# Kernel tuning notes

Hardware: AMD Instinct MI355X
Metric: run time of the kernel (lower is better)

The kernel has to match this reference:

```python
import jax, jax.numpy as jnp
import numpy as np

NC, NV = 1, 256
DE, D, DA = 512, 512, 512
KS = (2, 4, 4)
STRIDE = (2, 4, 4)
BLOCK = (4, 8, 8)
NHEAD = 8
NLAYERS = 2
PAD = -1
N_SLICE = STRIDE[0] * STRIDE[1] * STRIDE[2]  # 32


def _block_local_attention(x, wq, wk, wv, wo, block, n_head):
    # x: (b, d, T, H, W); non-overlapping block-local multi-head self-attention
    b, d, T, H, W = x.shape
    bt, bh, bw = block
    nt, nh, nw = T // bt, H // bh, W // bw
    L = bt * bh * bw
    da = wq.shape[1]
    hd = da // n_head
    # partition grid into blocks -> (b*nblocks, L, d)
    xs = x.transpose(0, 2, 3, 4, 1)                      # (b,T,H,W,d)
    xs = xs.reshape(b, nt, bt, nh, bh, nw, bw, d)
    xs = xs.transpose(0, 1, 3, 5, 2, 4, 6, 7).reshape(b * nt * nh * nw, L, d)
    q = (xs @ wq).reshape(-1, L, n_head, hd)
    k = (xs @ wk).reshape(-1, L, n_head, hd)
    v = (xs @ wv).reshape(-1, L, n_head, hd)
    scores = jnp.einsum('nqhd,nkhd->nhqk', q, k) / jnp.sqrt(jnp.float32(hd))
    attn = jax.nn.softmax(scores, axis=-1)
    o = jnp.einsum('nhqk,nkhd->nqhd', attn, v).reshape(-1, L, da)
    out = xs + o @ wo                                    # residual
    out = out.reshape(b, nt, nh, nw, bt, bh, bw, d)
    out = out.transpose(0, 1, 4, 2, 5, 3, 6, 7).reshape(b, T, H, W, d)
    return out.transpose(0, 4, 1, 2, 3)


def setup_inputs() -> dict:
    key = jax.random.key(0)
    ks = jax.random.split(key, 10)
    s = 0.02
    x = jax.random.randint(ks[0], (4, NC, 16, 64, 64), 0, NV)
    slice_idx = jax.random.randint(ks[1], (4,), 0, N_SLICE)
    conv_w = jax.random.normal(ks[2], (DE, NC * NV, *KS), jnp.float32) * s
    conv_b = jax.random.normal(ks[3], (DE,), jnp.float32) * s
    slice_emb = jax.random.normal(ks[4], (N_SLICE, DE), jnp.float32) * s
    proj_w = jax.random.normal(ks[5], (D, DE), jnp.float32) * s
    attn_wq = jax.random.normal(ks[6], (NLAYERS, D, DA), jnp.float32) * s
    attn_wk = jax.random.normal(ks[7], (NLAYERS, D, DA), jnp.float32) * s
    attn_wv = jax.random.normal(ks[8], (NLAYERS, D, DA), jnp.float32) * s
    attn_wo = jax.random.normal(ks[9], (NLAYERS, DA, D), jnp.float32) * s
    return {"x": x, "slice_idx": slice_idx, "conv_w": conv_w, "conv_b": conv_b,
            "slice_emb": slice_emb, "proj_w": proj_w, "attn_wq": attn_wq,
            "attn_wk": attn_wk, "attn_wv": attn_wv, "attn_wo": attn_wo}


def reference(x, slice_idx, conv_w, conv_b, slice_emb, proj_w,
              attn_wq, attn_wk, attn_wv, attn_wo):
    mask = x == PAD                                        # (b,nc,T,H,W)
    xt = jnp.where(mask, 0, x)
    oh = jax.nn.one_hot(xt, NV, dtype=jnp.float32)         # (b,nc,T,H,W,nv)
    oh = oh * (~mask)[..., None].astype(jnp.float32)
    b, nc, T, H, W, nv = oh.shape
    h = oh.transpose(0, 1, 5, 2, 3, 4).reshape(b, nc * nv, T, H, W)
    h = jax.lax.conv_general_dilated(h, conv_w, STRIDE, 'VALID',
                                     dimension_numbers=('NCDHW', 'OIDHW', 'NCDHW'))
    h = h + conv_b[None, :, None, None, None]
    h = h + slice_emb[slice_idx][:, :, None, None, None]
    h = jnp.einsum('bcthw,dc->bdthw', h, proj_w)           # 1x1x1 conv, no bias
    for i in range(NLAYERS):
        h = _block_local_attention(h, attn_wq[i], attn_wk[i], attn_wv[i],
                                   attn_wo[i], BLOCK, NHEAD)
    return h
```

## Files before the change

### kernel.cpp

```cpp
#include <hip/hip_runtime.h>
#include <hip/hip_bf16.h>

typedef unsigned short u16x8 __attribute__((ext_vector_type(8)));
typedef unsigned int u32x4 __attribute__((ext_vector_type(4)));
typedef __bf16 bf16x8 __attribute__((ext_vector_type(8)));
typedef float f32x4 __attribute__((ext_vector_type(4)));
typedef float f32x16 __attribute__((ext_vector_type(16)));

#define NTAP 32
#define NROWS 8192

__device__ inline unsigned short bf16bits(float f) {
  __hip_bfloat16 hb = __float2bfloat16(f);
  return __builtin_bit_cast(unsigned short, hb);
}
__device__ inline unsigned int pk2(float lo, float hi) {
  return (unsigned int)bf16bits(lo) | ((unsigned int)bf16bits(hi) << 16);
}
__device__ inline float bf2f(unsigned short u) {
  return __builtin_bit_cast(float, (unsigned int)u << 16);
}

__global__ void k_prepconv(const float* __restrict__ src, unsigned short* __restrict__ dst) {
  __shared__ float tile[64][65];
  int vt0 = blockIdx.x * 64, de0 = blockIdx.y * 64;
  int t = threadIdx.x;
#pragma unroll
  for (int p = 0; p < 16; p++) {
    int r = p * 4 + (t >> 6), c = t & 63;
    tile[r][c] = src[(size_t)(de0 + r) * 8192 + vt0 + c];
  }
  __syncthreads();
#pragma unroll
  for (int p = 0; p < 16; p++) {
    int r = p * 4 + (t >> 6), c = t & 63;
    dst[(size_t)(vt0 + r) * 512 + de0 + c] = bf16bits(tile[c][r]);
  }
}

__global__ void k_prepw(const float* __restrict__ proj_w, const float* __restrict__ wq,
                        const float* __restrict__ wk, const float* __restrict__ wv,
                        const float* __restrict__ wo, unsigned short* __restrict__ Wb) {
  __shared__ float tile[64][65];
  int mat = blockIdx.z;
  int n0 = blockIdx.x * 64, k0 = blockIdx.y * 64;
  int t = threadIdx.x;
  unsigned short* dst = Wb + (size_t)mat * 262144;
  if (mat == 0) {
#pragma unroll
    for (int p = 0; p < 16; p++) {
      int r = p * 4 + (t >> 6), c = t & 63;
      dst[(size_t)(n0 + r) * 512 + k0 + c] = bf16bits(proj_w[(size_t)(n0 + r) * 512 + k0 + c]);
    }
  } else {
    int idx = mat - 1, comp = idx & 3, L = idx >> 2;
    const float* srcs[4] = {wq, wk, wv, wo};
    const float* src = srcs[comp] + (size_t)L * 262144;
#pragma unroll
    for (int p = 0; p < 16; p++) {
      int r = p * 4 + (t >> 6), c = t & 63;
      tile[r][c] = src[(size_t)(k0 + r) * 512 + n0 + c];
    }
    __syncthreads();
#pragma unroll
    for (int p = 0; p < 16; p++) {
      int r = p * 4 + (t >> 6), c = t & 63;
      dst[(size_t)(n0 + r) * 512 + k0 + c] = bf16bits(tile[c][r]);
    }
  }
}

__global__ void k_embed(const int* __restrict__ x, const int* __restrict__ slice_idx,
                        const unsigned short* __restrict__ wTb, const float* __restrict__ conv_b,
                        const float* __restrict__ slice_emb, unsigned short* __restrict__ H0b) {
  int tid = threadIdx.x;
  int g = tid >> 6, l = tid & 63;
  int r = blockIdx.x * 4 + g;
  int blk = r >> 8, ll = r & 255;
  int bw = blk & 1, bh = (blk >> 1) & 1, bt = (blk >> 2) & 1, b = blk >> 3;
  int lw = ll & 7, lh = (ll >> 3) & 7, lt = ll >> 6;
  int t = bt * 4 + lt, h = bh * 8 + lh, w = bw * 8 + lw;

  __shared__ int toks[4][NTAP];
  if (l < NTAP) {
    int kt = l >> 4, kh = (l >> 2) & 3, kw = l & 3;
    toks[g][l] = x[((b * 16 + (2 * t + kt)) * 64 + (4 * h + kh)) * 64 + (4 * w + kw)];
  }
  __syncthreads();
  int sl = slice_idx[b];
  float4 cb0 = *(const float4*)&conv_b[l * 8];
  float4 cb1 = *(const float4*)&conv_b[l * 8 + 4];
  float4 se0 = *(const float4*)&slice_emb[sl * 512 + l * 8];
  float4 se1 = *(const float4*)&slice_emb[sl * 512 + l * 8 + 4];
  float acc[8] = {cb0.x + se0.x, cb0.y + se0.y, cb0.z + se0.z, cb0.w + se0.w,
                  cb1.x + se1.x, cb1.y + se1.y, cb1.z + se1.z, cb1.w + se1.w};
  for (int tap = 0; tap < NTAP; tap++) {
    int v = toks[g][tap];
    if (v >= 0) {
      u16x8 wv = *(const u16x8*)&wTb[(size_t)(v * NTAP + tap) * 512 + l * 8];
#pragma unroll
      for (int j = 0; j < 8; j++) acc[j] += bf2f(wv[j]);
    }
  }
  u16x8 o;
#pragma unroll
  for (int j = 0; j < 8; j++) o[j] = bf16bits(acc[j]);
  *(u16x8*)&H0b[(size_t)r * 512 + l * 8] = o;
}

template <int WM, bool RES>
__global__ void __launch_bounds__(256)
k_gemm_mfma(const unsigned short* __restrict__ A, const unsigned short* __restrict__ B,
            float* __restrict__ Cf, unsigned short* __restrict__ Cb,
            unsigned short* __restrict__ Vt) {
  __shared__ __align__(16) unsigned short As[128 * 64];
  __shared__ __align__(16) unsigned short Bs[128 * 64];
  int m0 = blockIdx.x * 128, n0 = blockIdx.y * 128;
  int tid = threadIdx.x;
  int lane = tid & 63, wid = tid >> 6;
  int wr = wid >> 1, wc = wid & 1;
  int l15 = lane & 15, lgrp = lane >> 4;
  int srow = tid >> 3, sx = tid & 7;
  f32x4 acc[4][4] = {};
  for (int k0 = 0; k0 < 512; k0 += 64) {
    u16x8 ra[4], rb[4];
#pragma unroll
    for (int i = 0; i < 4; i++) {
      int row = i * 32 + srow;
      int c = sx ^ (row & 7);
      ra[i] = *(const u16x8*)&A[(size_t)(m0 + row) * 512 + k0 + c * 8];
      rb[i] = *(const u16x8*)&B[(size_t)(n0 + row) * 512 + k0 + c * 8];
    }
    __syncthreads();
#pragma unroll
    for (int i = 0; i < 4; i++) {
      int row = i * 32 + srow;
      *(u16x8*)&As[row * 64 + sx * 8] = ra[i];
      *(u16x8*)&Bs[row * 64 + sx * 8] = rb[i];
    }
    __syncthreads();
#pragma unroll
    for (int kk = 0; kk < 2; kk++) {
      bf16x8 a[4], b[4];
#pragma unroll
      for (int m = 0; m < 4; m++) {
        int row = wr * 64 + m * 16 + l15;
        int xx = (kk * 4 + lgrp) ^ (row & 7);
        a[m] = __builtin_bit_cast(bf16x8, *(const u16x8*)&As[row * 64 + xx * 8]);
      }
#pragma unroll
      for (int n = 0; n < 4; n++) {
        int row = wc * 64 + n * 16 + l15;
        int xx = (kk * 4 + lgrp) ^ (row & 7);
        b[n] = __builtin_bit_cast(bf16x8, *(const u16x8*)&Bs[row * 64 + xx * 8]);
      }
#pragma unroll
      for (int m = 0; m < 4; m++)
#pragma unroll
        for (int n = 0; n < 4; n++)
          acc[m][n] = __builtin_amdgcn_mfma_f32_16x16x32_bf16(a[m], b[n], acc[m][n], 0, 0, 0);
    }
  }
#pragma unroll
  for (int m = 0; m < 4; m++) {
#pragma unroll
    for (int n = 0; n < 4; n++) {
      int gcol = n0 + wc * 64 + n * 16 + l15;
#pragma unroll
      for (int r = 0; r < 4; r++) {
        int grow = m0 + wr * 64 + m * 16 + lgrp * 4 + r;
        float v = acc[m][n][r];
        if (WM == 1) {
          if (RES) v += Cf[(size_t)grow * 512 + gcol];
          Cf[(size_t)grow * 512 + gcol] = v;
          Cb[(size_t)grow * 512 + gcol] = bf16bits(v);
        } else {
          if (gcol < 1024) Cb[(size_t)grow * 1024 + gcol] = bf16bits(v);
          else Vt[(size_t)(gcol - 1024) * 8192 + grow] = bf16bits(v);
        }
      }
    }
  }
}

__global__ void __launch_bounds__(256)
k_attn_mfma(const unsigned short* __restrict__ QKb, const unsigned short* __restrict__ Vt,
            unsigned short* __restrict__ O16) {
  __shared__ __align__(16) unsigned short Ks[256 * 64];
  __shared__ __align__(16) unsigned short Vs[64 * 256];
  int bid = blockIdx.x >> 3, head = blockIdx.x & 7;
  int r0 = bid * 256;
  int tid = threadIdx.x, lane = tid & 63, wid = tid >> 6;
  {
    int key = tid >> 3, j = tid & 7;
#pragma unroll
    for (int p = 0; p < 8; p++) {
      int k2 = key + p * 32;
      u16x8 v = *(const u16x8*)&QKb[(size_t)(r0 + k2) * 1024 + 512 + head * 64 + j * 8];
      *(u16x8*)&Ks[k2 * 64 + ((j ^ (k2 & 7)) * 8)] = v;
    }
    int dv = tid >> 2, sg = tid & 3;
    const unsigned short* src = &Vt[(size_t)(head * 64 + dv) * 8192 + r0 + sg * 64];
#pragma unroll
    for (int c = 0; c < 8; c++) {
      u16x8 v = *(const u16x8*)&src[c * 8];
      int ch = sg * 8 + c;
      *(u16x8*)&Vs[dv * 256 + ((ch ^ (dv & 7)) * 8)] = v;
    }
  }
  int l31 = lane & 31, hi = lane >> 5;
  int qb = wid * 64;
  bf16x8 qfrag[2][4];
#pragma unroll
  for (int g = 0; g < 2; g++)
#pragma unroll
    for (int s = 0; s < 4; s++)
      qfrag[g][s] = __builtin_bit_cast(
          bf16x8, *(const u16x8*)&QKb[(size_t)(r0 + qb + g * 32 + l31) * 1024 + head * 64 +
                                      s * 16 + hi * 8]);
  __syncthreads();

  f32x16 oacc[2][2] = {};
  float mx[2] = {-1e30f, -1e30f}, lsum[2] = {0.f, 0.f};

  for (int kt = 0; kt < 8; kt++) {
    bf16x8 kfrag[4];
    int key = kt * 32 + l31;
#pragma unroll
    for (int s = 0; s < 4; s++) {
      int j = s * 2 + hi;
      kfrag[s] = __builtin_bit_cast(bf16x8, *(const u16x8*)&Ks[key * 64 + ((j ^ (key & 7)) * 8)]);
    }
#pragma unroll
    for (int g = 0; g < 2; g++) {
      f32x16 sacc = {};
#pragma unroll
      for (int s = 0; s < 4; s++)
        sacc = __builtin_amdgcn_mfma_f32_32x32x16_bf16(kfrag[s], qfrag[g][s], sacc, 0, 0, 0);
      float tmax = sacc[0];
#pragma unroll
      for (int r = 1; r < 16; r++) tmax = fmaxf(tmax, sacc[r]);
      tmax = fmaxf(tmax, __shfl_xor(tmax, 32, 64));
      float mn = fmaxf(mx[g], tmax);
      float sc = __expf((mx[g] - mn) * 0.125f);
      float p[16], ts = 0.f;
#pragma unroll
      for (int r = 0; r < 16; r++) {
        p[r] = __expf((sacc[r] - mn) * 0.125f);
        ts += p[r];
      }
      ts += __shfl_xor(ts, 32, 64);
      lsum[g] = lsum[g] * sc + ts;
      mx[g] = mn;
#pragma unroll
      for (int dvt = 0; dvt < 2; dvt++)
#pragma unroll
        for (int r = 0; r < 16; r++) oacc[g][dvt][r] *= sc;
#pragma unroll
      for (int st = 0; st < 2; st++) {
        unsigned int A = pk2(p[st * 8 + 0], p[st * 8 + 1]);
        unsigned int Bw = pk2(p[st * 8 + 2], p[st * 8 + 3]);
        unsigned int C = pk2(p[st * 8 + 4], p[st * 8 + 5]);
        unsigned int D = pk2(p[st * 8 + 6], p[st * 8 + 7]);
        asm volatile("v_permlane32_swap_b32 %0, %1" : "+v"(A), "+v"(C));
        asm volatile("v_permlane32_swap_b32 %0, %1" : "+v"(Bw), "+v"(D));
        u32x4 fw = {A, Bw, C, D};
        bf16x8 pfrag = __builtin_bit_cast(bf16x8, fw);
#pragma unroll
        for (int dvt = 0; dvt < 2; dvt++) {
          int dv = dvt * 32 + l31;
          int ch = kt * 4 + st * 2 + hi;
          bf16x8 vfrag = __builtin_bit_cast(
              bf16x8, *(const u16x8*)&Vs[dv * 256 + ((ch ^ (dv & 7)) * 8)]);
          oacc[g][dvt] = __builtin_amdgcn_mfma_f32_32x32x16_bf16(vfrag, pfrag, oacc[g][dvt], 0, 0, 0);
        }
      }
    }
  }
#pragma unroll
  for (int g = 0; g < 2; g++) {
    float inv = 1.f / lsum[g];
    size_t rowb = (size_t)(r0 + qb + g * 32 + l31) * 512 + head * 64;
#pragma unroll
    for (int dvt = 0; dvt < 2; dvt++)
#pragma unroll
      for (int r = 0; r < 16; r += 2) {
        int dv = dvt * 32 + (r & 3) + 8 * (r >> 2) + 4 * hi;
        unsigned int po = pk2(oacc[g][dvt][r] * inv, oacc[g][dvt][r + 1] * inv);
        *(unsigned int*)&O16[rowb + dv] = po;
      }
  }
}

__global__ void k_writeout(const float* __restrict__ H, float* __restrict__ out) {
  __shared__ float t[512][33];
  int bp = blockIdx.x;
  int d0 = blockIdx.y * 32;
  int tid = threadIdx.x;
  int base_row = bp * 512;
#pragma unroll
  for (int i = 0; i < 16; i++) {
    int id = i * 256 + tid;
    int r = id >> 3, c = id & 7;
    float4 v = *(const float4*)&H[(size_t)(base_row + r) * 512 + d0 + c * 4];
    t[r][c * 4 + 0] = v.x;
    t[r][c * 4 + 1] = v.y;
    t[r][c * 4 + 2] = v.z;
    t[r][c * 4 + 3] = v.w;
  }
  __syncthreads();
  int b = bp >> 2, bt = (bp >> 1) & 1, bh = bp & 1;
  int w = tid & 15, lh = (tid >> 4) & 7, ltl = tid >> 7;
  int lw = w & 7, bw = w >> 3;
#pragma unroll
  for (int dd = 0; dd < 32; dd++) {
#pragma unroll
    for (int s = 0; s < 2; s++) {
      int lt = s * 2 + ltl;
      int pos = bw * 256 + lt * 64 + lh * 8 + lw;
      out[((size_t)(b * 512 + d0 + dd) * 8 + bt * 4 + lt) * 256 + (bh * 8 + lh) * 16 + w] =
          t[pos][dd];
    }
  }
}

extern "C" void kernel_launch(void* const* d_in, const int* in_sizes, int n_in,
                              void* d_out, int out_size, void* d_ws, size_t ws_size,
                              hipStream_t stream) {
  const int* x = (const int*)d_in[0];
  const int* slice_idx = (const int*)d_in[1];
  const float* conv_w = (const float*)d_in[2];
  const float* conv_b = (const float*)d_in[3];
  const float* slice_emb = (const float*)d_in[4];
  const float* proj_w = (const float*)d_in[5];
  const float* wq = (const float*)d_in[6];
  const float* wk = (const float*)d_in[7];
  const float* wv = (const float*)d_in[8];
  const float* wo = (const float*)d_in[9];
  float* out = (float*)d_out;

  float* ws = (float*)d_ws;
  unsigned short* wTb = (unsigned short*)ws;
  float* H = ws + 4194304;
  unsigned short* H0b = (unsigned short*)(ws + 8388608);
  unsigned short* Hb = (unsigned short*)(ws + 10485760);
  unsigned short* Ob16 = (unsigned short*)(ws + 12582912);
  unsigned short* QKb = (unsigned short*)(ws + 14680064);
  unsigned short* Vt = (unsigned short*)(ws + 18874368);
  unsigned short* Wb = (unsigned short*)(ws + 20971520);

  k_prepconv<<<dim3(128, 8), 256, 0, stream>>>(conv_w, wTb);
  k_prepw<<<dim3(8, 8, 9), 256, 0, stream>>>(proj_w, wq, wk, wv, wo, Wb);
  k_embed<<<2048, 256, 0, stream>>>(x, slice_idx, wTb, conv_b, slice_emb, H0b);
  k_gemm_mfma<1, false><<<dim3(64, 4), 256, 0, stream>>>(H0b, Wb, H, Hb, nullptr);

  for (int L = 0; L < 2; L++) {
    k_gemm_mfma<2, false><<<dim3(64, 12), 256, 0, stream>>>(
        Hb, Wb + (size_t)262144 * (1 + 4 * L), nullptr, QKb, Vt);
    k_attn_mfma<<<256, 256, 0, stream>>>(QKb, Vt, Ob16);
    k_gemm_mfma<1, true><<<dim3(64, 4), 256, 0, stream>>>(
        Ob16, Wb + (size_t)262144 * (4 + 4 * L), H, Hb, nullptr);
  }
  k_writeout<<<dim3(16, 16), 256, 0, stream>>>(H, out);
}
```

Measured before the change: 267.5 us.

## Merge weight prep kernels, coalesce V-transpose stores, split attention queries across blocks

Folds the two weight-preparation kernels into one launch to cut a kernel launch. In the QKV GEMM, the V output tiles are now transposed through shared memory (reusing the A/B staging buffers via a union) so Vt is written with 16-byte coalesced stores instead of scattered 2-byte stores. The attention kernel now splits each block's 256 queries across two workgroups (512 blocks instead of 256), each wave handling 32 queries. This improves CU occupancy on a 256-CU device, at the cost of loading K/V into LDS twice per head-block.

```diff
diff --git a/kernel.cpp b/kernel.cpp
--- a/kernel.cpp
+++ b/kernel.cpp
@@ -21,51 +21,52 @@
   return __builtin_bit_cast(float, (unsigned int)u << 16);
 }
 
-__global__ void k_prepconv(const float* __restrict__ src, unsigned short* __restrict__ dst) {
+__global__ void k_prep(const float* __restrict__ conv_w, const float* __restrict__ proj_w,
+                       const float* __restrict__ wq, const float* __restrict__ wk,
+                       const float* __restrict__ wv, const float* __restrict__ wo,
+                       unsigned short* __restrict__ wTb, unsigned short* __restrict__ Wb) {
   __shared__ float tile[64][65];
-  int vt0 = blockIdx.x * 64, de0 = blockIdx.y * 64;
+  int bid = blockIdx.x;
   int t = threadIdx.x;
-#pragma unroll
-  for (int p = 0; p < 16; p++) {
-    int r = p * 4 + (t >> 6), c = t & 63;
-    tile[r][c] = src[(size_t)(de0 + r) * 8192 + vt0 + c];
-  }
-  __syncthreads();
-#pragma unroll
-  for (int p = 0; p < 16; p++) {
-    int r = p * 4 + (t >> 6), c = t & 63;
-    dst[(size_t)(vt0 + r) * 512 + de0 + c] = bf16bits(tile[c][r]);
-  }
-}
-
-__global__ void k_prepw(const float* __restrict__ proj_w, const float* __restrict__ wq,
-                        const float* __restrict__ wk, const float* __restrict__ wv,
-                        const float* __restrict__ wo, unsigned short* __restrict__ Wb) {
-  __shared__ float tile[64][65];
-  int mat = blockIdx.z;
-  int n0 = blockIdx.x * 64, k0 = blockIdx.y * 64;
-  int t = threadIdx.x;
-  unsigned short* dst = Wb + (size_t)mat * 262144;
-  if (mat == 0) {
+  if (bid < 1024) {
+    int vt0 = (bid & 127) * 64, de0 = (bid >> 7) * 64;
 #pragma unroll
     for (int p = 0; p < 16; p++) {
       int r = p * 4 + (t >> 6), c = t & 63;
-      dst[(size_t)(n0 + r) * 512 + k0 + c] = bf16bits(proj_w[(size_t)(n0 + r) * 512 + k0 + c]);
-    }
-  } else {
-    int idx = mat - 1, comp = idx & 3, L = idx >> 2;
-    const float* srcs[4] = {wq, wk, wv, wo};
-    const float* src = srcs[comp] + (size_t)L * 262144;
+      tile[r][c] = conv_w[(size_t)(de0 + r) * 8192 + vt0 + c];
+    }
+    __syncthreads();
 #pragma unroll
     for (int p = 0; p < 16; p++) {
       int r = p * 4 + (t >> 6), c = t & 63;
-      tile[r][c] = src[(size_t)(k0 + r) * 512 + n0 + c];
-    }
-    __syncthreads();
-#pragma unroll
-    for (int p = 0; p < 16; p++) {
-      int r = p * 4 + (t >> 6), c = t & 63;
-      dst[(size_t)(n0 + r) * 512 + k0 + c] = bf16bits(tile[c][r]);
+      wTb[(size_t)(vt0 + r) * 512 + de0 + c] = bf16bits(tile[c][r]);
+    }
+  } else {
+    int wid2 = bid - 1024;
+    int mat = wid2 >> 6, rem = wid2 & 63;
+    int n0 = (rem & 7) * 64, k0 = (rem >> 3) * 64;
+    unsigned short* dst = Wb + (size_t)mat * 262144;
+    if (mat == 0) {
+#pragma unroll
+      for (int p = 0; p < 16; p++) {
+        int r = p * 4 + (t >> 6), c = t & 63;
+        dst[(size_t)(n0 + r) * 512 + k0 + c] = bf16bits(proj_w[(size_t)(n0 + r) * 512 + k0 + c]);
+      }
+    } else {
+      int idx = mat - 1, comp = idx & 3, L = idx >> 2;
+      const float* srcs[4] = {wq, wk, wv, wo};
+      const float* src = srcs[comp] + (size_t)L * 262144;
+#pragma unroll
+      for (int p = 0; p < 16; p++) {
+        int r = p * 4 + (t >> 6), c = t & 63;
+        tile[r][c] = src[(size_t)(k0 + r) * 512 + n0 + c];
+      }
+      __syncthreads();
+#pragma unroll
+      for (int p = 0; p < 16; p++) {
+        int r = p * 4 + (t >> 6), c = t & 63;
+        dst[(size_t)(n0 + r) * 512 + k0 + c] = bf16bits(tile[c][r]);
+      }
     }
   }
 }
@@ -113,8 +114,11 @@
 k_gemm_mfma(const unsigned short* __restrict__ A, const unsigned short* __restrict__ B,
             float* __restrict__ Cf, unsigned short* __restrict__ Cb,
             unsigned short* __restrict__ Vt) {
-  __shared__ __align__(16) unsigned short As[128 * 64];
-  __shared__ __align__(16) unsigned short Bs[128 * 64];
+  struct ABb { unsigned short As[128 * 64]; unsigned short Bs[128 * 64]; };
+  union SMu { ABb ab; unsigned short T[64][136]; };
+  __shared__ __align__(16) SMu sm;
+  unsigned short* As = sm.ab.As;
+  unsigned short* Bs = sm.ab.Bs;
   int m0 = blockIdx.x * 128, n0 = blockIdx.y * 128;
   int tid = threadIdx.x;
   int lane = tid & 63, wid = tid >> 6;
@@ -161,6 +165,31 @@
           acc[m][n] = __builtin_amdgcn_mfma_f32_16x16x32_bf16(a[m], b[n], acc[m][n], 0, 0, 0);
     }
   }
+  if (WM == 2 && n0 >= 1024) {
+    __syncthreads();
+#pragma unroll
+    for (int p = 0; p < 2; p++) {
+      if (wc == p) {
+#pragma unroll
+        for (int m = 0; m < 4; m++)
+#pragma unroll
+          for (int n = 0; n < 4; n++)
+#pragma unroll
+            for (int r = 0; r < 4; r++)
+              sm.T[n * 16 + l15][wr * 64 + m * 16 + lgrp * 4 + r] = bf16bits(acc[m][n][r]);
+      }
+      __syncthreads();
+      int c = tid >> 2, rcb = tid & 3;
+#pragma unroll
+      for (int it = 0; it < 4; it++) {
+        int rc = it * 4 + rcb;
+        *(u16x8*)&Vt[(size_t)(n0 - 1024 + p * 64 + c) * 8192 + m0 + rc * 8] =
+            *(const u16x8*)&sm.T[c][rc * 8];
+      }
+      if (p == 0) __syncthreads();
+    }
+    return;
+  }
 #pragma unroll
   for (int m = 0; m < 4; m++) {
 #pragma unroll
@@ -175,8 +204,7 @@
           Cf[(size_t)grow * 512 + gcol] = v;
           Cb[(size_t)grow * 512 + gcol] = bf16bits(v);
         } else {
-          if (gcol < 1024) Cb[(size_t)grow * 1024 + gcol] = bf16bits(v);
-          else Vt[(size_t)(gcol - 1024) * 8192 + grow] = bf16bits(v);
+          Cb[(size_t)grow * 1024 + gcol] = bf16bits(v);
         }
       }
     }
@@ -188,7 +216,8 @@
             unsigned short* __restrict__ O16) {
   __shared__ __align__(16) unsigned short Ks[256 * 64];
   __shared__ __align__(16) unsigned short Vs[64 * 256];
-  int bid = blockIdx.x >> 3, head = blockIdx.x & 7;
+  int xg = blockIdx.x;
+  int bid = xg >> 4, head = (xg >> 1) & 7, qh = xg & 1;
   int r0 = bid * 256;
   int tid = threadIdx.x, lane = tid & 63, wid = tid >> 6;
   {
@@ -209,19 +238,16 @@
     }
   }
   int l31 = lane & 31, hi = lane >> 5;
-  int qb = wid * 64;
-  bf16x8 qfrag[2][4];
-#pragma unroll
-  for (int g = 0; g < 2; g++)
-#pragma unroll
-    for (int s = 0; s < 4; s++)
-      qfrag[g][s] = __builtin_bit_cast(
-          bf16x8, *(const u16x8*)&QKb[(size_t)(r0 + qb + g * 32 + l31) * 1024 + head * 64 +
-                                      s * 16 + hi * 8]);
+  int q = r0 + qh * 128 + wid * 32 + l31;
+  bf16x8 qfrag[4];
+#pragma unroll
+  for (int s = 0; s < 4; s++)
+    qfrag[s] = __builtin_bit_cast(
+        bf16x8, *(const u16x8*)&QKb[(size_t)q * 1024 + head * 64 + s * 16 + hi * 8]);
   __syncthreads();
 
-  f32x16 oacc[2][2] = {};
-  float mx[2] = {-1e30f, -1e30f}, lsum[2] = {0.f, 0.f};
+  f32x16 oacc[2] = {};
+  float mx = -1e30f, lsum = 0.f;
 
   for (int kt = 0; kt < 8; kt++) {
     bf16x8 kfrag[4];
@@ -231,65 +257,59 @@
       int j = s * 2 + hi;
       kfrag[s] = __builtin_bit_cast(bf16x8, *(const u16x8*)&Ks[key * 64 + ((j ^ (key & 7)) * 8)]);
     }
-#pragma unroll
-    for (int g = 0; g < 2; g++) {
-      f32x16 sacc = {};
-#pragma unroll
-      for (int s = 0; s < 4; s++)
-        sacc = __builtin_amdgcn_mfma_f32_32x32x16_bf16(kfrag[s], qfrag[g][s], sacc, 0, 0, 0);
-      float tmax = sacc[0];
-#pragma unroll
-      for (int r = 1; r < 16; r++) tmax = fmaxf(tmax, sacc[r]);
-      tmax = fmaxf(tmax, __shfl_xor(tmax, 32, 64));
-      float mn = fmaxf(mx[g], tmax);
-      float sc = __expf((mx[g] - mn) * 0.125f);
-      float p[16], ts = 0.f;
-#pragma unroll
-      for (int r = 0; r < 16; r++) {
-        p[r] = __expf((sacc[r] - mn) * 0.125f);
-        ts += p[r];
-      }
-      ts += __shfl_xor(ts, 32, 64);
-      lsum[g] = lsum[g] * sc + ts;
-      mx[g] = mn;
-#pragma unroll
-      for (int dvt = 0; dvt < 2; dvt++)
-#pragma unroll
-        for (int r = 0; r < 16; r++) oacc[g][dvt][r] *= sc;
-#pragma unroll
-      for (int st = 0; st < 2; st++) {
-        unsigned int A = pk2(p[st * 8 + 0], p[st * 8 + 1]);
-        unsigned int Bw = pk2(p[st * 8 + 2], p[st * 8 + 3]);
-        unsigned int C = pk2(p[st * 8 + 4], p[st * 8 + 5]);
-        unsigned int D = pk2(p[st * 8 + 6], p[st * 8 + 7]);
-        asm volatile("v_permlane32_swap_b32 %0, %1" : "+v"(A), "+v"(C));
-        asm volatile("v_permlane32_swap_b32 %0, %1" : "+v"(Bw), "+v"(D));
-        u32x4 fw = {A, Bw, C, D};
-        bf16x8 pfrag = __builtin_bit_cast(bf16x8, fw);
-#pragma unroll
-        for (int dvt = 0; dvt < 2; dvt++) {
-          int dv = dvt * 32 + l31;
-          int ch = kt * 4 + st * 2 + hi;
-          bf16x8 vfrag = __builtin_bit_cast(
-              bf16x8, *(const u16x8*)&Vs[dv * 256 + ((ch ^ (dv & 7)) * 8)]);
-          oacc[g][dvt] = __builtin_amdgcn_mfma_f32_32x32x16_bf16(vfrag, pfrag, oacc[g][dvt], 0, 0, 0);
-        }
-      }
-    }
-  }
-#pragma unroll
-  for (int g = 0; g < 2; g++) {
-    float inv = 1.f / lsum[g];
-    size_t rowb = (size_t)(r0 + qb + g * 32 + l31) * 512 + head * 64;
+    f32x16 sacc = {};
+#pragma unroll
+    for (int s = 0; s < 4; s++)
+      sacc = __builtin_amdgcn_mfma_f32_32x32x16_bf16(kfrag[s], qfrag[s], sacc, 0, 0, 0);
+    float tmax = sacc[0];
+#pragma unroll
+    for (int r = 1; r < 16; r++) tmax = fmaxf(tmax, sacc[r]);
+    tmax = fmaxf(tmax, __shfl_xor(tmax, 32, 64));
+    float mn = fmaxf(mx, tmax);
+    float sc = __expf((mx - mn) * 0.125f);
+    float p[16], ts = 0.f;
+#pragma unroll
+    for (int r = 0; r < 16; r++) {
+      p[r] = __expf((sacc[r] - mn) * 0.125f);
+      ts += p[r];
+    }
+    ts += __shfl_xor(ts, 32, 64);
+    lsum = lsum * sc + ts;
+    mx = mn;
 #pragma unroll
     for (int dvt = 0; dvt < 2; dvt++)
 #pragma unroll
-      for (int r = 0; r < 16; r += 2) {
-        int dv = dvt * 32 + (r & 3) + 8 * (r >> 2) + 4 * hi;
-        unsigned int po = pk2(oacc[g][dvt][r] * inv, oacc[g][dvt][r + 1] * inv);
-        *(unsigned int*)&O16[rowb + dv] = po;
-      }
-  }
+      for (int r = 0; r < 16; r++) oacc[dvt][r] *= sc;
+#pragma unroll
+    for (int st = 0; st < 2; st++) {
+      unsigned int Aw = pk2(p[st * 8 + 0], p[st * 8 + 1]);
+      unsigned int Bw = pk2(p[st * 8 + 2], p[st * 8 + 3]);
+      unsigned int Cw = pk2(p[st * 8 + 4], p[st * 8 + 5]);
+      unsigned int Dw = pk2(p[st * 8 + 6], p[st * 8 + 7]);
+      asm volatile("v_permlane32_swap_b32 %0, %1" : "+v"(Aw), "+v"(Cw));
+      asm volatile("v_permlane32_swap_b32 %0, %1" : "+v"(Bw), "+v"(Dw));
+      u32x4 fw = {Aw, Bw, Cw, Dw};
+      bf16x8 pfrag = __builtin_bit_cast(bf16x8, fw);
+#pragma unroll
+      for (int dvt = 0; dvt < 2; dvt++) {
+        int dv = dvt * 32 + l31;
+        int ch = kt * 4 + st * 2 + hi;
+        bf16x8 vfrag = __builtin_bit_cast(
+            bf16x8, *(const u16x8*)&Vs[dv * 256 + ((ch ^ (dv & 7)) * 8)]);
+        oacc[dvt] = __builtin_amdgcn_mfma_f32_32x32x16_bf16(vfrag, pfrag, oacc[dvt], 0, 0, 0);
+      }
+    }
+  }
+  float inv = 1.f / lsum;
+  size_t rowb = (size_t)q * 512 + head * 64;
+#pragma unroll
+  for (int dvt = 0; dvt < 2; dvt++)
+#pragma unroll
+    for (int r = 0; r < 16; r += 2) {
+      int dv = dvt * 32 + (r & 3) + 8 * (r >> 2) + 4 * hi;
+      unsigned int po = pk2(oacc[dvt][r] * inv, oacc[dvt][r + 1] * inv);
+      *(unsigned int*)&O16[rowb + dv] = po;
+    }
 }
 
 __global__ void k_writeout(const float* __restrict__ H, float* __restrict__ out) {
@@ -349,15 +369,14 @@
   unsigned short* Vt = (unsigned short*)(ws + 18874368);
   unsigned short* Wb = (unsigned short*)(ws + 20971520);
 
-  k_prepconv<<<dim3(128, 8), 256, 0, stream>>>(conv_w, wTb);
-  k_prepw<<<dim3(8, 8, 9), 256, 0, stream>>>(proj_w, wq, wk, wv, wo, Wb);
+  k_prep<<<1600, 256, 0, stream>>>(conv_w, proj_w, wq, wk, wv, wo, wTb, Wb);
   k_embed<<<2048, 256, 0, stream>>>(x, slice_idx, wTb, conv_b, slice_emb, H0b);
   k_gemm_mfma<1, false><<<dim3(64, 4), 256, 0, stream>>>(H0b, Wb, H, Hb, nullptr);
 
   for (int L = 0; L < 2; L++) {
     k_gemm_mfma<2, false><<<dim3(64, 12), 256, 0, stream>>>(
         Hb, Wb + (size_t)262144 * (1 + 4 * L), nullptr, QKb, Vt);
-    k_attn_mfma<<<256, 256, 0, stream>>>(QKb, Vt, Ob16);
+    k_attn_mfma<<<512, 256, 0, stream>>>(QKb, Vt, Ob16);
     k_gemm_mfma<1, true><<<dim3(64, 4), 256, 0, stream>>>(
         Ob16, Wb + (size_t)262144 * (4 + 4 * L), H, Hb, nullptr);
   }
```

After: 265.8 us. About the same (-0.6%).
